# Performance work log

Measured on AMD Instinct MI355X. Metric: run time of the kernel, lower is better.

Reference implementation:

```python
import jax, jax.numpy as jnp
import numpy as np
from jax import lax

_A = -0.75  # PyTorch bicubic coefficient


def _cubic_kernel(x):
    x = np.abs(x)
    return np.where(x <= 1.0, (_A + 2) * x**3 - (_A + 3) * x**2 + 1,
                    np.where(x < 2.0, _A * x**3 - 5 * _A * x**2 + 8 * _A * x - 4 * _A, 0.0))


def _cubic_mat(out_s, in_s):
    # align_corners=True bicubic interpolation matrix [out_s, in_s]
    i = np.arange(out_s)
    s = i * (in_s - 1) / (out_s - 1) if out_s > 1 else np.zeros(out_s)
    f = np.floor(s).astype(np.int64)
    t = s - f
    M = np.zeros((out_s, in_s), dtype=np.float32)
    for off in range(-1, 3):
        idx = np.clip(f + off, 0, in_s - 1)
        np.add.at(M, (i, idx), _cubic_kernel(t - off).astype(np.float32))
    return jnp.asarray(M)


def _bicubic_up(x, out_hw):
    Mh = _cubic_mat(out_hw[0], x.shape[-2])
    Mw = _cubic_mat(out_hw[1], x.shape[-1])
    y = jnp.einsum('Hh,bchw->bcHw', Mh, x)
    return jnp.einsum('Ww,bcHw->bcHW', Mw, y)


def _conv(x, w, b, pad=1):
    y = lax.conv_general_dilated(x, w, (1, 1), [(pad, pad), (pad, pad)],
                                 dimension_numbers=('NCHW', 'OIHW', 'NCHW'))
    return y + b[None, :, None, None]


def _pool(x):
    return lax.reduce_window(x, -jnp.inf, lax.max, (1, 1, 2, 2), (1, 1, 2, 2), 'VALID')


def _features(x, ws):
    # VGG19 feat1 = conv0+relu (64ch, full res); feat2 = conv2..conv14 (256ch, 1/4 res)
    x1 = jax.nn.relu(_conv(x, *ws[0]))
    h = jax.nn.relu(_conv(x1, *ws[1]))
    h = _pool(h)
    h = jax.nn.relu(_conv(h, *ws[2]))
    h = jax.nn.relu(_conv(h, *ws[3]))
    h = _pool(h)
    h = jax.nn.relu(_conv(h, *ws[4]))
    h = jax.nn.relu(_conv(h, *ws[5]))
    h = jax.nn.relu(_conv(h, *ws[6]))
    h = _bicubic_up(h, x1.shape[-2:])  # bicubic, align_corners=True
    return jnp.concatenate([x1, h], axis=1)  # 64 + 256 = 320 channels


def _forward(x_ref, x_template, w0, b0, w2, b2, w5, b5, w7, b7, w10, b10, w12, b12,
             w14, b14, coef_ref, coef_temp, fw1, fb1, fw2, fb2, fw3, fb3):
    ws = [(w0, b0), (w2, b2), (w5, b5), (w7, b7), (w10, b10), (w12, b12), (w14, b14)]
    fref = _features(x_ref, ws)
    ftem = _features(x_template, ws)
    # L2-normalize over channel dim
    fref = fref / (1e-8 + jnp.linalg.norm(fref, axis=1, keepdims=True))
    ftem = ftem / (1e-8 + jnp.linalg.norm(ftem, axis=1, keepdims=True))
    b, c, H, W = fref.shape
    fref = fref.reshape(b, c, H // 2, 2, W // 2, 2).mean(axis=(3, 5))
    # dense correlation volume
    dist = jnp.einsum('bcmn,bcpq->bmnpq', fref, ftem) / 320.0
    m, n, p, q = dist.shape[1:]
    dist = dist.reshape(b, m * n, p * q)
    # dual-axis softmax + sqrt combination (LoFTR-style)
    conf_ref = jax.nn.softmax(coef_ref * dist, axis=-2)
    conf_tmp = jax.nn.softmax(coef_temp * dist, axis=-1)
    confidence = jnp.sqrt(conf_ref * conf_tmp)
    conf_values, _ = lax.top_k(confidence, 5)  # [b, m*n, 5]
    conf = conf_values.reshape(b, m, n, 5).transpose(0, 3, 1, 2)
    # final head (dropout = identity in eval)
    h = jax.nn.relu(_conv(conf, fw1, fb1))
    h = jax.nn.relu(_conv(h, fw2, fb2))
    out = _conv(h, fw3, fb3, pad=0)
    out = _bicubic_up(out, x_ref.shape[-2:])
    return out


def setup_inputs() -> dict:
    key = jax.random.key(0)
    ks = jax.random.split(key, 16)
    B, H, W = 1, 128, 128

    def cw(k, o, i, s):
        return jax.random.normal(k, (o, i, s, s), jnp.float32) * (1.0 / np.sqrt(i * s * s))

    d = {
        'x_ref': jax.random.normal(ks[0], (B, 3, H, W), jnp.float32),
        'x_template': jax.random.normal(ks[1], (B, 3, H, W), jnp.float32),
        'w0': cw(ks[2], 64, 3, 3), 'b0': jnp.zeros((64,), jnp.float32),
        'w2': cw(ks[3], 64, 64, 3), 'b2': jnp.zeros((64,), jnp.float32),
        'w5': cw(ks[4], 128, 64, 3), 'b5': jnp.zeros((128,), jnp.float32),
        'w7': cw(ks[5], 128, 128, 3), 'b7': jnp.zeros((128,), jnp.float32),
        'w10': cw(ks[6], 256, 128, 3), 'b10': jnp.zeros((256,), jnp.float32),
        'w12': cw(ks[7], 256, 256, 3), 'b12': jnp.zeros((256,), jnp.float32),
        'w14': cw(ks[8], 256, 256, 3), 'b14': jnp.zeros((256,), jnp.float32),
        'coef_ref': jnp.float32(1.0), 'coef_temp': jnp.float32(1.0),
        # final head: weights_init_normal -> N(1/3, 0.02)
        'fw1': 1.0 / 3 + 0.02 * jax.random.normal(ks[9], (8, 5, 3, 3), jnp.float32),
        'fb1': 0.02 * jax.random.normal(ks[10], (8,), jnp.float32),
        'fw2': 1.0 / 3 + 0.02 * jax.random.normal(ks[11], (8, 8, 3, 3), jnp.float32),
        'fb2': 0.02 * jax.random.normal(ks[12], (8,), jnp.float32),
        'fw3': 1.0 / 3 + 0.02 * jax.random.normal(ks[13], (1, 8, 1, 1), jnp.float32),
        'fb3': 0.02 * jax.random.normal(ks[14], (1,), jnp.float32),
    }
    return d


def reference(x_ref, x_template, w0, b0, w2, b2, w5, b5, w7, b7, w10, b10, w12, b12,
              w14, b14, coef_ref, coef_temp, fw1, fb1, fw2, fb2, fw3, fb3):
    return _forward(x_ref, x_template, w0, b0, w2, b2, w5, b5, w7, b7, w10, b10,
                    w12, b12, w14, b14, coef_ref, coef_temp, fw1, fb1, fw2, fb2, fw3, fb3)
```

## Files before the change

kernel.cpp:

```cpp
#include <hip/hip_runtime.h>
#include <math.h>

typedef unsigned short ushort_t;
typedef unsigned int uint_t;
typedef __attribute__((ext_vector_type(8))) short bf16x8;
typedef __attribute__((ext_vector_type(4))) float f32x4;

#define FSTRIDE ((size_t)16384 * 320)
#define TSTRIDE ((size_t)16384 * 64)

__device__ inline ushort_t f2bf(float f) {
    union { float f; uint_t u; } x; x.f = f;
    uint_t r = x.u + 0x7fffu + ((x.u >> 16) & 1u);
    return (ushort_t)(r >> 16);
}
__device__ inline float bf2f(ushort_t h) {
    union { uint_t u; float f; } x; x.u = ((uint_t)h) << 16;
    return x.f;
}
__device__ inline float bflo(uint_t u) {
    union { uint_t u; float f; } x; x.u = u << 16; return x.f;
}
__device__ inline float bfhi(uint_t u) {
    union { uint_t u; float f; } x; x.u = u & 0xffff0000u; return x.f;
}
__device__ inline uint_t cvtpk_bf16(float lo, float hi) {
    uint_t r;
    asm volatile("v_cvt_pk_bf16_f32 %0, %1, %2" : "=v"(r) : "v"(lo), "v"(hi));
    return r;
}
__device__ inline void gload16(const void* g, void* l) {
    __builtin_amdgcn_global_load_lds(
        (const __attribute__((address_space(1))) void*)g,
        (__attribute__((address_space(3))) void*)l, 16, 0, 0);
}

__global__ void wtrans_k(const float* __restrict__ w, ushort_t* __restrict__ wT, int CO, int CI)
{
    int idx = blockIdx.x * 256 + threadIdx.x;
    if (idx >= CO * CI * 9) return;
    int tap = idx % 9;
    int rem = idx / 9;
    int ci = rem % CI;
    int co = rem / CI;
    wT[((size_t)tap * CO + co) * CI + ci] = f2bf(w[idx]);
}

__global__ __launch_bounds__(256) void conv0_k(const float* __restrict__ x0, const float* __restrict__ x1,
                                               const float* __restrict__ w,
                                               const float* __restrict__ b, ushort_t* __restrict__ F)
{
    const float* x = blockIdx.y ? x1 : x0;
    F += (size_t)blockIdx.y * FSTRIDE;
    int co = threadIdx.x & 63;
    int p = blockIdx.x * 4 + (threadIdx.x >> 6);
    int y = p >> 7, xx = p & 127;
    float acc = b[co];
#pragma unroll
    for (int ci = 0; ci < 3; ++ci) {
#pragma unroll
        for (int t = 0; t < 9; ++t) {
            int dy = t / 3 - 1, dx = t % 3 - 1;
            int yy = y + dy, xc = xx + dx;
            if ((unsigned)yy < 128u && (unsigned)xc < 128u) {
                acc += x[ci * 16384 + yy * 128 + xc] * w[co * 27 + ci * 9 + t];
            }
        }
    }
    F[(size_t)p * 320 + co] = f2bf(fmaxf(acc, 0.f));
}

template<int CI>
__global__ __launch_bounds__(256) void conv_mfma_k(
    const ushort_t* __restrict__ in, int ldin, int inoff, size_t inImgStride,
    const ushort_t* __restrict__ wT, const float* __restrict__ bias,
    ushort_t* __restrict__ out, int ldout, int outoff, size_t outImgStride,
    int H, int W, int CO)
{
    in += (size_t)blockIdx.z * inImgStride;
    out += (size_t)blockIdx.z * outImgStride;
    const int tid = threadIdx.x;
    const int lane = tid & 63, wid = tid >> 6;
    const int wr = wid >> 1, wc = wid & 1;
    const int m0 = blockIdx.x * 64;
    const int n0 = blockIdx.y * 64;
    const int fr = lane & 15;
    const int fo = (lane >> 4) << 3;

    size_t abase[2];
    unsigned vmask[2];
#pragma unroll
    for (int mi = 0; mi < 2; ++mi) {
        int p = m0 + wr * 32 + mi * 16 + fr;
        int y = p / W, x = p % W;
        abase[mi] = (size_t)p * ldin + inoff + fo;
        unsigned vm = 0;
#pragma unroll
        for (int t = 0; t < 9; ++t) {
            int dy = t / 3 - 1, dx = t % 3 - 1;
            if ((unsigned)(y + dy) < (unsigned)H && (unsigned)(x + dx) < (unsigned)W) vm |= 1u << t;
        }
        vmask[mi] = vm;
    }

    f32x4 zero = {0.f, 0.f, 0.f, 0.f};
    f32x4 acc[2][2] = {{zero, zero}, {zero, zero}};
    const bf16x8 zz = {0, 0, 0, 0, 0, 0, 0, 0};

    for (int t = 0; t < 9; ++t) {
        int toff = ((t / 3 - 1) * W + (t % 3 - 1)) * ldin;
        bool v0 = (vmask[0] >> t) & 1u;
        bool v1 = (vmask[1] >> t) & 1u;
        const ushort_t* wp0 = wT + ((size_t)(t * CO + n0 + wc * 32 + fr)) * CI + fo;
        const ushort_t* wp1 = wp0 + (size_t)16 * CI;
#pragma unroll
        for (int kc = 0; kc < CI / 32; ++kc) {
            int k0 = kc * 32;
            bf16x8 a0 = v0 ? *(const bf16x8*)(in + abase[0] + toff + k0) : zz;
            bf16x8 a1 = v1 ? *(const bf16x8*)(in + abase[1] + toff + k0) : zz;
            bf16x8 b0 = *(const bf16x8*)(wp0 + k0);
            bf16x8 b1 = *(const bf16x8*)(wp1 + k0);
            acc[0][0] = __builtin_amdgcn_mfma_f32_16x16x32_bf16(b0, a0, acc[0][0], 0, 0, 0);
            acc[0][1] = __builtin_amdgcn_mfma_f32_16x16x32_bf16(b1, a0, acc[0][1], 0, 0, 0);
            acc[1][0] = __builtin_amdgcn_mfma_f32_16x16x32_bf16(b0, a1, acc[1][0], 0, 0, 0);
            acc[1][1] = __builtin_amdgcn_mfma_f32_16x16x32_bf16(b1, a1, acc[1][1], 0, 0, 0);
        }
    }

#pragma unroll
    for (int mi = 0; mi < 2; ++mi) {
#pragma unroll
        for (int ni = 0; ni < 2; ++ni) {
            int pix = m0 + wr * 32 + mi * 16 + (lane & 15);
            int ch = n0 + wc * 32 + ni * 16 + ((lane >> 4) << 2);
            float4 bv = *(const float4*)(bias + ch);
            float r0 = fmaxf(acc[mi][ni][0] + bv.x, 0.f);
            float r1 = fmaxf(acc[mi][ni][1] + bv.y, 0.f);
            float r2 = fmaxf(acc[mi][ni][2] + bv.z, 0.f);
            float r3 = fmaxf(acc[mi][ni][3] + bv.w, 0.f);
            uint2 pk;
            pk.x = (uint_t)f2bf(r0) | ((uint_t)f2bf(r1) << 16);
            pk.y = (uint_t)f2bf(r2) | ((uint_t)f2bf(r3) << 16);
            *(uint2*)(out + (size_t)pix * ldout + outoff + ch) = pk;
        }
    }
}

template<int CI>
__global__ __launch_bounds__(64) void conv_mfma1w_k(
    const ushort_t* __restrict__ in, int ldin, size_t inImgStride,
    const ushort_t* __restrict__ wT, const float* __restrict__ bias,
    ushort_t* __restrict__ out, int ldout, size_t outImgStride,
    int H, int W, int CO)
{
    in += (size_t)blockIdx.z * inImgStride;
    out += (size_t)blockIdx.z * outImgStride;
    const int lane = threadIdx.x;
    const int m0 = blockIdx.x * 32;
    const int n0 = blockIdx.y * 32;
    const int fr = lane & 15;
    const int fo = (lane >> 4) << 3;

    size_t abase[2];
    unsigned vmask[2];
#pragma unroll
    for (int mi = 0; mi < 2; ++mi) {
        int p = m0 + mi * 16 + fr;
        int y = p / W, x = p % W;
        abase[mi] = (size_t)p * ldin + fo;
        unsigned vm = 0;
#pragma unroll
        for (int t = 0; t < 9; ++t) {
            int dy = t / 3 - 1, dx = t % 3 - 1;
            if ((unsigned)(y + dy) < (unsigned)H && (unsigned)(x + dx) < (unsigned)W) vm |= 1u << t;
        }
        vmask[mi] = vm;
    }

    f32x4 zero = {0.f, 0.f, 0.f, 0.f};
    f32x4 acc[2][2] = {{zero, zero}, {zero, zero}};
    const bf16x8 zz = {0, 0, 0, 0, 0, 0, 0, 0};

    for (int t = 0; t < 9; ++t) {
        int toff = ((t / 3 - 1) * W + (t % 3 - 1)) * ldin;
        bool v0 = (vmask[0] >> t) & 1u;
        bool v1 = (vmask[1] >> t) & 1u;
        const ushort_t* wp0 = wT + ((size_t)(t * CO + n0 + fr)) * CI + fo;
        const ushort_t* wp1 = wp0 + (size_t)16 * CI;
#pragma unroll
        for (int kc = 0; kc < CI / 32; ++kc) {
            int k0 = kc * 32;
            bf16x8 a0 = v0 ? *(const bf16x8*)(in + abase[0] + toff + k0) : zz;
            bf16x8 a1 = v1 ? *(const bf16x8*)(in + abase[1] + toff + k0) : zz;
            bf16x8 b0 = *(const bf16x8*)(wp0 + k0);
            bf16x8 b1 = *(const bf16x8*)(wp1 + k0);
            acc[0][0] = __builtin_amdgcn_mfma_f32_16x16x32_bf16(b0, a0, acc[0][0], 0, 0, 0);
            acc[0][1] = __builtin_amdgcn_mfma_f32_16x16x32_bf16(b1, a0, acc[0][1], 0, 0, 0);
            acc[1][0] = __builtin_amdgcn_mfma_f32_16x16x32_bf16(b0, a1, acc[1][0], 0, 0, 0);
            acc[1][1] = __builtin_amdgcn_mfma_f32_16x16x32_bf16(b1, a1, acc[1][1], 0, 0, 0);
        }
    }

#pragma unroll
    for (int mi = 0; mi < 2; ++mi) {
#pragma unroll
        for (int ni = 0; ni < 2; ++ni) {
            int pix = m0 + mi * 16 + (lane & 15);
            int ch = n0 + ni * 16 + ((lane >> 4) << 2);
            float4 bv = *(const float4*)(bias + ch);
            float r0 = fmaxf(acc[mi][ni][0] + bv.x, 0.f);
            float r1 = fmaxf(acc[mi][ni][1] + bv.y, 0.f);
            float r2 = fmaxf(acc[mi][ni][2] + bv.z, 0.f);
            float r3 = fmaxf(acc[mi][ni][3] + bv.w, 0.f);
            uint2 pk;
            pk.x = (uint_t)f2bf(r0) | ((uint_t)f2bf(r1) << 16);
            pk.y = (uint_t)f2bf(r2) | ((uint_t)f2bf(r3) << 16);
            *(uint2*)(out + (size_t)pix * ldout + ch) = pk;
        }
    }
}

__global__ void maxpool_nhwc_k(const ushort_t* __restrict__ in, ushort_t* __restrict__ out,
                               int C, int Hi, int Wi)
{
    in += (size_t)blockIdx.y * TSTRIDE;
    out += (size_t)blockIdx.y * TSTRIDE;
    int idx = blockIdx.x * 256 + threadIdx.x;
    int CG = C >> 3;
    int Wo = Wi >> 1, Ho = Hi >> 1;
    if (idx >= Ho * Wo * CG) return;
    int cg = idx % CG;
    int p = idx / CG;
    int y = p / Wo, x = p % Wo;
    const ushort_t* ip = in + ((size_t)(2 * y) * Wi + 2 * x) * C + cg * 8;
    bf16x8 v0 = *(const bf16x8*)(ip);
    bf16x8 v1 = *(const bf16x8*)(ip + C);
    bf16x8 v2 = *(const bf16x8*)(ip + (size_t)Wi * C);
    bf16x8 v3 = *(const bf16x8*)(ip + (size_t)Wi * C + C);
    bf16x8 r;
#pragma unroll
    for (int j = 0; j < 8; ++j) {
        float m = fmaxf(fmaxf(bf2f((ushort_t)v0[j]), bf2f((ushort_t)v1[j])),
                        fmaxf(bf2f((ushort_t)v2[j]), bf2f((ushort_t)v3[j])));
        r[j] = (short)f2bf(m);
    }
    *(bf16x8*)(out + (size_t)p * C + cg * 8) = r;
}

__device__ inline void cubw(float t, float* w) {
    float x0 = 1.f + t, x2 = 1.f - t, x3 = 2.f - t;
    w[0] = ((-0.75f*x0 + 3.75f)*x0 - 6.f)*x0 + 3.f;
    w[1] = (1.25f*t - 2.25f)*t*t + 1.f;
    w[2] = (1.25f*x2 - 2.25f)*x2*x2 + 1.f;
    w[3] = ((-0.75f*x3 + 3.75f)*x3 - 6.f)*x3 + 3.f;
}

__global__ __launch_bounds__(256) void bicubic_nhwc_k(const ushort_t* __restrict__ in, ushort_t* __restrict__ F)
{
    in += (size_t)blockIdx.y * TSTRIDE;
    F += (size_t)blockIdx.y * FSTRIDE;
    int idx = blockIdx.x * 256 + threadIdx.x;
    int cg = idx & 31;
    int p = idx >> 5;
    int Y = p >> 7, X = p & 127;
    float sy = (float)Y * (31.f / 127.f);
    float sx = (float)X * (31.f / 127.f);
    int fy = (int)floorf(sy), fx = (int)floorf(sx);
    float ty = sy - (float)fy, tx = sx - (float)fx;
    float wy[4], wx[4];
    cubw(ty, wy); cubw(tx, wx);
    float a[8] = {0.f, 0.f, 0.f, 0.f, 0.f, 0.f, 0.f, 0.f};
#pragma unroll
    for (int i = 0; i < 4; ++i) {
        int yy = min(max(fy - 1 + i, 0), 31);
#pragma unroll
        for (int j = 0; j < 4; ++j) {
            int xx = min(max(fx - 1 + j, 0), 31);
            float w = wy[i] * wx[j];
            bf16x8 v = *(const bf16x8*)(in + ((size_t)yy * 32 + xx) * 256 + cg * 8);
#pragma unroll
            for (int e = 0; e < 8; ++e) a[e] += w * bf2f((ushort_t)v[e]);
        }
    }
    bf16x8 r;
#pragma unroll
    for (int e = 0; e < 8; ++e) r[e] = (short)f2bf(a[e]);
    *(bf16x8*)(F + (size_t)p * 320 + 64 + cg * 8) = r;
}

__global__ __launch_bounds__(256) void norm_k(ushort_t* __restrict__ F)
{
    int lane = threadIdx.x & 63;
    int p = blockIdx.x * 4 + (threadIdx.x >> 6);
    ushort_t* rp = F + (size_t)p * 320;
    bool act = lane < 40;
    bf16x8 v = {0, 0, 0, 0, 0, 0, 0, 0};
    float ss = 0.f;
    if (act) {
        v = *(const bf16x8*)(rp + lane * 8);
#pragma unroll
        for (int e = 0; e < 8; ++e) { float f = bf2f((ushort_t)v[e]); ss += f * f; }
    }
#pragma unroll
    for (int off = 32; off > 0; off >>= 1) ss += __shfl_xor(ss, off);
    float inv = 1.f / (1e-8f + sqrtf(ss));
    if (act) {
#pragma unroll
        for (int e = 0; e < 8; ++e) v[e] = (short)f2bf(bf2f((ushort_t)v[e]) * inv);
        *(bf16x8*)(rp + lane * 8) = v;
    }
}

__global__ void pool_ref_nhwc_k(const ushort_t* __restrict__ F, ushort_t* __restrict__ A)
{
    int idx = blockIdx.x * 256 + threadIdx.x;
    if (idx >= 4096 * 40) return;
    int cg = idx % 40;
    int m = idx / 40;
    int y = m >> 6, x = m & 63;
    const ushort_t* ip = F + ((size_t)(2 * y) * 128 + 2 * x) * 320 + cg * 8;
    bf16x8 v0 = *(const bf16x8*)(ip);
    bf16x8 v1 = *(const bf16x8*)(ip + 320);
    bf16x8 v2 = *(const bf16x8*)(ip + 128 * 320);
    bf16x8 v3 = *(const bf16x8*)(ip + 128 * 320 + 320);
    bf16x8 r;
#pragma unroll
    for (int j = 0; j < 8; ++j) {
        float s = bf2f((ushort_t)v0[j]) + bf2f((ushort_t)v1[j]) + bf2f((ushort_t)v2[j]) + bf2f((ushort_t)v3[j]);
        r[j] = (short)f2bf(0.25f * s);
    }
    *(bf16x8*)(A + (size_t)m * 320 + cg * 8) = r;
}

__global__ __launch_bounds__(256) void gemm_corr_k(
    const ushort_t* __restrict__ A, const ushort_t* __restrict__ B, ushort_t* __restrict__ D,
    const float* __restrict__ coefr, const float* __restrict__ coeft,
    float* __restrict__ rpsum, float* __restrict__ cpsum)
{
    __shared__ ushort_t lA[128 * 32];
    __shared__ ushort_t lB[128 * 32];
    __shared__ float cl[2][128];
    __shared__ float rl[2][128];
    const int tid = threadIdx.x;
    const int lane = tid & 63;
    const int wid = tid >> 6;
    const int wr = wid >> 1, wc = wid & 1;
    const int m0 = blockIdx.y * 128, n0 = blockIdx.x * 128;
    const int fr = lane & 15;
    const int fo = (lane >> 4) << 3;
    const int srow = tid >> 2;
    const int scol = (tid & 3) << 3;

    const ushort_t* Ag0 = A + (size_t)(m0 + srow) * 320 + scol;
    const ushort_t* Ag1 = Ag0 + (size_t)64 * 320;
    const ushort_t* Bg0 = B + (size_t)(n0 + srow) * 320 + scol;
    const ushort_t* Bg1 = Bg0 + (size_t)64 * 320;
    ushort_t* lA0 = lA + wid * 512;
    ushort_t* lA1 = lA + 2048 + wid * 512;
    ushort_t* lB0 = lB + wid * 512;
    ushort_t* lB1 = lB + 2048 + wid * 512;

    f32x4 zero = {0.f, 0.f, 0.f, 0.f};
    f32x4 acc[4][4];
#pragma unroll
    for (int i = 0; i < 4; ++i)
#pragma unroll
        for (int j = 0; j < 4; ++j) acc[i][j] = zero;

    for (int k0 = 0; k0 < 320; k0 += 32) {
        gload16(Ag0 + k0, lA0);
        gload16(Ag1 + k0, lA1);
        gload16(Bg0 + k0, lB0);
        gload16(Bg1 + k0, lB1);
        __syncthreads();
        bf16x8 af[4], bfr[4];
#pragma unroll
        for (int mi = 0; mi < 4; ++mi)
            af[mi] = *(const bf16x8*)&lA[(wr * 64 + mi * 16 + fr) * 32 + fo];
#pragma unroll
        for (int ni = 0; ni < 4; ++ni)
            bfr[ni] = *(const bf16x8*)&lB[(wc * 64 + ni * 16 + fr) * 32 + fo];
#pragma unroll
        for (int mi = 0; mi < 4; ++mi)
#pragma unroll
            for (int ni = 0; ni < 4; ++ni)
                acc[mi][ni] = __builtin_amdgcn_mfma_f32_16x16x32_bf16(bfr[ni], af[mi], acc[mi][ni], 0, 0, 0);
        __syncthreads();
    }

    const float s = 1.0f / 320.0f;
    const float cr = coefr[0], ct = coeft[0];
    const bool sameCoef = (cr == ct);
    float rpx[4] = {0.f, 0.f, 0.f, 0.f};
    float cpx[4][4];
#pragma unroll
    for (int ni = 0; ni < 4; ++ni)
#pragma unroll
        for (int r = 0; r < 4; ++r) cpx[ni][r] = 0.f;

    const int mrow = lane & 15;
    const int ng = (lane >> 4) << 2;
#pragma unroll
    for (int mi = 0; mi < 4; ++mi) {
        int m = m0 + wr * 64 + mi * 16 + mrow;
        ushort_t* drow = D + (size_t)m * 16384;
#pragma unroll
        for (int ni = 0; ni < 4; ++ni) {
            int n = n0 + wc * 64 + ni * 16 + ng;
            float d0 = acc[mi][ni][0] * s;
            float d1 = acc[mi][ni][1] * s;
            float d2 = acc[mi][ni][2] * s;
            float d3 = acc[mi][ni][3] * s;
            uint2 pk;
            pk.x = cvtpk_bf16(d0, d1);
            pk.y = cvtpk_bf16(d2, d3);
            *(uint2*)(drow + n) = pk;
            float e0 = __expf(cr * d0), e1 = __expf(cr * d1);
            float e2 = __expf(cr * d2), e3 = __expf(cr * d3);
            cpx[ni][0] += e0; cpx[ni][1] += e1; cpx[ni][2] += e2; cpx[ni][3] += e3;
            if (sameCoef) {
                rpx[mi] += e0 + e1 + e2 + e3;
            } else {
                rpx[mi] += __expf(ct * d0) + __expf(ct * d1) + __expf(ct * d2) + __expf(ct * d3);
            }
        }
    }
#pragma unroll
    for (int mi = 0; mi < 4; ++mi) {
        rpx[mi] += __shfl_xor(rpx[mi], 16);
        rpx[mi] += __shfl_xor(rpx[mi], 32);
    }
    if (lane < 16) {
#pragma unroll
        for (int mi = 0; mi < 4; ++mi)
            rl[wc][wr * 64 + mi * 16 + lane] = rpx[mi];
    }
#pragma unroll
    for (int ni = 0; ni < 4; ++ni)
#pragma unroll
        for (int r = 0; r < 4; ++r) {
            cpx[ni][r] += __shfl_xor(cpx[ni][r], 1);
            cpx[ni][r] += __shfl_xor(cpx[ni][r], 2);
            cpx[ni][r] += __shfl_xor(cpx[ni][r], 4);
            cpx[ni][r] += __shfl_xor(cpx[ni][r], 8);
        }
    if ((lane & 15) == 0) {
        int g = lane >> 4;
#pragma unroll
        for (int ni = 0; ni < 4; ++ni)
#pragma unroll
            for (int r = 0; r < 4; ++r)
                cl[wr][wc * 64 + ni * 16 + g * 4 + r] = cpx[ni][r];
    }
    __syncthreads();
    if (tid < 128) {
        cpsum[(size_t)blockIdx.y * 16384 + n0 + tid] = cl[0][tid] + cl[1][tid];
        rpsum[(size_t)blockIdx.x * 4096 + m0 + tid] = rl[0][tid] + rl[1][tid];
    }
}

__global__ void colfin_k(const float* __restrict__ cpsum, float* __restrict__ lc)
{
    int j = blockIdx.x * 256 + threadIdx.x;
    float s = 0.f;
#pragma unroll
    for (int k = 0; k < 32; ++k) s += cpsum[(size_t)k * 16384 + j];
    lc[j] = -0.5f * __logf(s);
}
__global__ void rowfin_k(const float* __restrict__ rpsum, float* __restrict__ invr)
{
    int m = blockIdx.x * 256 + threadIdx.x;
    float s = 0.f;
#pragma unroll
    for (int k = 0; k < 128; ++k) s += rpsum[(size_t)k * 4096 + m];
    invr[m] = rsqrtf(s);
}

#define INS5(w_) { float w = (w_); float mx; \
    mx = fmaxf(w, t0); w = fminf(w, t0); t0 = mx; \
    mx = fmaxf(w, t1); w = fminf(w, t1); t1 = mx; \
    mx = fmaxf(w, t2); w = fminf(w, t2); t2 = mx; \
    mx = fmaxf(w, t3); w = fminf(w, t3); t3 = mx; \
    t4 = fmaxf(w, t4); }

__global__ __launch_bounds__(256) void row_topk_k(
    const ushort_t* __restrict__ Dist, const float* __restrict__ lc,
    const float* __restrict__ invr,
    const float* __restrict__ coefr, const float* __restrict__ coeft,
    float* __restrict__ conf5)
{
    int wid = threadIdx.x >> 6, lane = threadIdx.x & 63;
    int row = blockIdx.x * 4 + wid;
    float hc = 0.5f * (coefr[0] + coeft[0]);
    const ushort_t* rp = Dist + (size_t)row * 16384;

    float t0 = -1e30f, t1 = -1e30f, t2 = -1e30f, t3 = -1e30f, t4 = -1e30f;
    for (int i = 0; i < 32; ++i) {
        int col = (i * 64 + lane) * 8;
        uint4 u = *(const uint4*)(rp + col);
        float4 l0 = *(const float4*)(lc + col);
        float4 l1 = *(const float4*)(lc + col + 4);
        INS5(fmaf(hc, bflo(u.x), l0.x));
        INS5(fmaf(hc, bfhi(u.x), l0.y));
        INS5(fmaf(hc, bflo(u.y), l0.z));
        INS5(fmaf(hc, bfhi(u.y), l0.w));
        INS5(fmaf(hc, bflo(u.z), l1.x));
        INS5(fmaf(hc, bfhi(u.z), l1.y));
        INS5(fmaf(hc, bflo(u.w), l1.z));
        INS5(fmaf(hc, bfhi(u.w), l1.w));
    }
#pragma unroll
    for (int off = 1; off < 64; off <<= 1) {
        float o0 = __shfl_xor(t0, off), o1 = __shfl_xor(t1, off), o2 = __shfl_xor(t2, off);
        float o3 = __shfl_xor(t3, off), o4 = __shfl_xor(t4, off);
        INS5(o0); INS5(o1); INS5(o2); INS5(o3); INS5(o4);
    }
    if (lane == 0) {
        float iv = invr[row];
        conf5[0 * 4096 + row] = __expf(t0) * iv;
        conf5[1 * 4096 + row] = __expf(t1) * iv;
        conf5[2 * 4096 + row] = __expf(t2) * iv;
        conf5[3 * 4096 + row] = __expf(t3) * iv;
        conf5[4 * 4096 + row] = __expf(t4) * iv;
    }
}

__global__ void conv3x3_k(const float* __restrict__ in, const float* __restrict__ wgt,
                          const float* __restrict__ bias, float* __restrict__ out,
                          int Cin, int H, int W, int relu)
{
    int p = blockIdx.x * 256 + threadIdx.x;
    int HW = H * W;
    if (p >= HW) return;
    int co0 = blockIdx.y * 8;
    int y = p / W, x = p - y * W;
    float acc0 = bias[co0+0], acc1 = bias[co0+1], acc2 = bias[co0+2], acc3 = bias[co0+3];
    float acc4 = bias[co0+4], acc5 = bias[co0+5], acc6 = bias[co0+6], acc7 = bias[co0+7];
    bool ym = y > 0, yp = y < H-1, xm = x > 0, xp = x < W-1;
    for (int ci = 0; ci < Cin; ++ci) {
        const float* ip = in + (size_t)ci * HW + p;
        float v0 = (ym && xm) ? ip[-W-1] : 0.f;
        float v1 = (ym)       ? ip[-W]   : 0.f;
        float v2 = (ym && xp) ? ip[-W+1] : 0.f;
        float v3 = (xm)       ? ip[-1]   : 0.f;
        float v4 =              ip[0];
        float v5 = (xp)       ? ip[1]    : 0.f;
        float v6 = (yp && xm) ? ip[W-1]  : 0.f;
        float v7 = (yp)       ? ip[W]    : 0.f;
        float v8 = (yp && xp) ? ip[W+1]  : 0.f;
        const float* wp = wgt + ((size_t)co0 * Cin + ci) * 9;
        size_t ws = (size_t)Cin * 9;
#define CACC(q, a) { const float* wq = wp + q * ws; \
        a += wq[0]*v0 + wq[1]*v1 + wq[2]*v2 + wq[3]*v3 + wq[4]*v4 \
           + wq[5]*v5 + wq[6]*v6 + wq[7]*v7 + wq[8]*v8; }
        CACC(0, acc0) CACC(1, acc1) CACC(2, acc2) CACC(3, acc3)
        CACC(4, acc4) CACC(5, acc5) CACC(6, acc6) CACC(7, acc7)
#undef CACC
    }
#define CW(q, a) { float r = a; if (relu) r = fmaxf(r, 0.f); out[(size_t)(co0+q)*HW + p] = r; }
    CW(0, acc0) CW(1, acc1) CW(2, acc2) CW(3, acc3)
    CW(4, acc4) CW(5, acc5) CW(6, acc6) CW(7, acc7)
#undef CW
}

__global__ void bicubic_k(const float* __restrict__ in, float* __restrict__ out,
                          int C, int Hin, int Win, int Hout, int Wout)
{
    int idx = blockIdx.x * 256 + threadIdx.x;
    int total = C * Hout * Wout;
    if (idx >= total) return;
    int X = idx % Wout;
    int Y = (idx / Wout) % Hout;
    int c = idx / (Wout * Hout);
    float sy = (float)Y * (float)(Hin - 1) / (float)(Hout - 1);
    float sx = (float)X * (float)(Win - 1) / (float)(Wout - 1);
    int fy = (int)floorf(sy), fx = (int)floorf(sx);
    float ty = sy - (float)fy, tx = sx - (float)fx;
    float wy[4], wx[4];
    cubw(ty, wy); cubw(tx, wx);
    const float* ip = in + (size_t)c * Hin * Win;
    float acc = 0.f;
#pragma unroll
    for (int i = 0; i < 4; ++i) {
        int yy = min(max(fy - 1 + i, 0), Hin - 1);
        float ra = 0.f;
#pragma unroll
        for (int j = 0; j < 4; ++j) {
            int xx = min(max(fx - 1 + j, 0), Win - 1);
            ra += wx[j] * ip[yy * Win + xx];
        }
        acc += wy[i] * ra;
    }
    out[idx] = acc;
}

__global__ void conv1x1_k(const float* __restrict__ in, const float* __restrict__ w,
                          const float* __restrict__ b, float* __restrict__ out, int Cin, int HW)
{
    int p = blockIdx.x * 256 + threadIdx.x;
    if (p >= HW) return;
    float a = b[0];
    for (int c = 0; c < Cin; ++c) a += w[c] * in[(size_t)c * HW + p];
    out[p] = a;
}

extern "C" void kernel_launch(void* const* d_in, const int* in_sizes, int n_in,
                              void* d_out, int out_size, void* d_ws, size_t ws_size,
                              hipStream_t stream)
{
    const float* x_ref = (const float*)d_in[0];
    const float* x_tem = (const float*)d_in[1];
    const float* w0  = (const float*)d_in[2];   const float* b0  = (const float*)d_in[3];
    const float* w2  = (const float*)d_in[4];   const float* b2  = (const float*)d_in[5];
    const float* w5  = (const float*)d_in[6];   const float* b5  = (const float*)d_in[7];
    const float* w7  = (const float*)d_in[8];   const float* b7  = (const float*)d_in[9];
    const float* w10 = (const float*)d_in[10];  const float* b10 = (const float*)d_in[11];
    const float* w12 = (const float*)d_in[12];  const float* b12 = (const float*)d_in[13];
    const float* w14 = (const float*)d_in[14];  const float* b14 = (const float*)d_in[15];
    const float* coefr = (const float*)d_in[16];
    const float* coeft = (const float*)d_in[17];
    const float* fw1 = (const float*)d_in[18];  const float* fb1 = (const float*)d_in[19];
    const float* fw2 = (const float*)d_in[20];  const float* fb2 = (const float*)d_in[21];
    const float* fw3 = (const float*)d_in[22];  const float* fb3 = (const float*)d_in[23];
    float* out = (float*)d_out;

    char* wsp = (char*)d_ws;
    auto alloc = [&](size_t bytes) { char* p = wsp; wsp += (bytes + 255) & ~(size_t)255; return p; };
    ushort_t* F     = (ushort_t*)alloc(2 * FSTRIDE * 2);
    ushort_t* t1    = (ushort_t*)alloc(2 * TSTRIDE * 2);
    ushort_t* t2    = (ushort_t*)alloc(2 * TSTRIDE * 2);
    ushort_t* wT2   = (ushort_t*)alloc((size_t)64 * 64 * 9 * 2);
    ushort_t* wT5   = (ushort_t*)alloc((size_t)128 * 64 * 9 * 2);
    ushort_t* wT7   = (ushort_t*)alloc((size_t)128 * 128 * 9 * 2);
    ushort_t* wT10  = (ushort_t*)alloc((size_t)256 * 128 * 9 * 2);
    ushort_t* wT12  = (ushort_t*)alloc((size_t)256 * 256 * 9 * 2);
    ushort_t* wT14  = (ushort_t*)alloc((size_t)256 * 256 * 9 * 2);
    ushort_t* Abuf  = (ushort_t*)alloc((size_t)4096 * 320 * 2);
    ushort_t* dist  = (ushort_t*)alloc((size_t)4096 * 16384 * 2);
    float*    rpsum = (float*)alloc((size_t)128 * 4096 * 4);
    float*    cpsum = (float*)alloc((size_t)32 * 16384 * 4);
    float*    lc    = (float*)alloc(16384 * 4);
    float*    invr  = (float*)alloc(4096 * 4);
    float*    conf5 = (float*)alloc(5 * 4096 * 4);
    float*    h1    = (float*)alloc(8 * 4096 * 4);
    float*    h2    = (float*)alloc(8 * 4096 * 4);
    float*    out64 = (float*)alloc(4096 * 4);
    (void)ws_size; (void)n_in; (void)in_sizes; (void)out_size;

    wtrans_k<<<(64*64*9 + 255)/256, 256, 0, stream>>>(w2, wT2, 64, 64);
    wtrans_k<<<(128*64*9 + 255)/256, 256, 0, stream>>>(w5, wT5, 128, 64);
    wtrans_k<<<(128*128*9 + 255)/256, 256, 0, stream>>>(w7, wT7, 128, 128);
    wtrans_k<<<(256*128*9 + 255)/256, 256, 0, stream>>>(w10, wT10, 256, 128);
    wtrans_k<<<(256*256*9 + 255)/256, 256, 0, stream>>>(w12, wT12, 256, 256);
    wtrans_k<<<(256*256*9 + 255)/256, 256, 0, stream>>>(w14, wT14, 256, 256);

    conv0_k<<<dim3(4096, 2), 256, 0, stream>>>(x_ref, x_tem, w0, b0, F);
    conv_mfma_k<64><<<dim3(256, 1, 2), 256, 0, stream>>>(F, 320, 0, FSTRIDE, wT2, b2, t1, 64, 0, TSTRIDE, 128, 128, 64);
    maxpool_nhwc_k<<<dim3(128, 2), 256, 0, stream>>>(t1, t2, 64, 128, 128);
    conv_mfma_k<64><<<dim3(64, 2, 2), 256, 0, stream>>>(t2, 64, 0, TSTRIDE, wT5, b5, t1, 128, 0, TSTRIDE, 64, 64, 128);
    conv_mfma_k<128><<<dim3(64, 2, 2), 256, 0, stream>>>(t1, 128, 0, TSTRIDE, wT7, b7, t2, 128, 0, TSTRIDE, 64, 64, 128);
    maxpool_nhwc_k<<<dim3(64, 2), 256, 0, stream>>>(t2, t1, 128, 64, 64);
    conv_mfma1w_k<128><<<dim3(32, 8, 2), 64, 0, stream>>>(t1, 128, TSTRIDE, wT10, b10, t2, 256, TSTRIDE, 32, 32, 256);
    conv_mfma1w_k<256><<<dim3(32, 8, 2), 64, 0, stream>>>(t2, 256, TSTRIDE, wT12, b12, t1, 256, TSTRIDE, 32, 32, 256);
    conv_mfma1w_k<256><<<dim3(32, 8, 2), 64, 0, stream>>>(t1, 256, TSTRIDE, wT14, b14, t2, 256, TSTRIDE, 32, 32, 256);
    bicubic_nhwc_k<<<dim3(2048, 2), 256, 0, stream>>>(t2, F);
    norm_k<<<8192, 256, 0, stream>>>(F);

    pool_ref_nhwc_k<<<640, 256, 0, stream>>>(F, Abuf);

    gemm_corr_k<<<dim3(128, 32), 256, 0, stream>>>(Abuf, F + FSTRIDE, dist, coefr, coeft, rpsum, cpsum);

    colfin_k<<<64, 256, 0, stream>>>(cpsum, lc);
    rowfin_k<<<16, 256, 0, stream>>>(rpsum, invr);

    row_topk_k<<<1024, 256, 0, stream>>>(dist, lc, invr, coefr, coeft, conf5);

    conv3x3_k<<<dim3(16, 1), 256, 0, stream>>>(conf5, fw1, fb1, h1, 5, 64, 64, 1);
    conv3x3_k<<<dim3(16, 1), 256, 0, stream>>>(h1, fw2, fb2, h2, 8, 64, 64, 1);
    conv1x1_k<<<16, 256, 0, stream>>>(h2, fw3, fb3, out64, 8, 4096);
    bicubic_k<<<64, 256, 0, stream>>>(out64, out, 1, 64, 64, 128, 128);
}
```

Baseline: 409.7 us.

## Double-buffer LDS in correlation GEMM and early-skip top-5 insertion in row scan

The correlation GEMM now uses two LDS buffers per operand and issues the global-to-LDS loads for the next K slice before running MFMAs on the current one. This removes one barrier per iteration and lets load latency overlap with compute, at the cost of doubling that kernel's shared memory. The row top-5 kernel first takes the max of each group of 8 candidates and skips the insertion network when that max cannot beat the current 5th best. Most groups should then need only a few compares instead of 8 insertions, though the new branch can diverge across lanes.

```diff
diff --git a/kernel.cpp b/kernel.cpp
--- a/kernel.cpp
+++ b/kernel.cpp
@@ -337,8 +337,8 @@
     const float* __restrict__ coefr, const float* __restrict__ coeft,
     float* __restrict__ rpsum, float* __restrict__ cpsum)
 {
-    __shared__ ushort_t lA[128 * 32];
-    __shared__ ushort_t lB[128 * 32];
+    __shared__ ushort_t lA[2][128 * 32];
+    __shared__ ushort_t lB[2][128 * 32];
     __shared__ float cl[2][128];
     __shared__ float rl[2][128];
     const int tid = threadIdx.x;
@@ -355,10 +355,6 @@
     const ushort_t* Ag1 = Ag0 + (size_t)64 * 320;
     const ushort_t* Bg0 = B + (size_t)(n0 + srow) * 320 + scol;
     const ushort_t* Bg1 = Bg0 + (size_t)64 * 320;
-    ushort_t* lA0 = lA + wid * 512;
-    ushort_t* lA1 = lA + 2048 + wid * 512;
-    ushort_t* lB0 = lB + wid * 512;
-    ushort_t* lB1 = lB + 2048 + wid * 512;
 
     f32x4 zero = {0.f, 0.f, 0.f, 0.f};
     f32x4 acc[4][4];
@@ -367,26 +363,38 @@
 #pragma unroll
         for (int j = 0; j < 4; ++j) acc[i][j] = zero;
 
-    for (int k0 = 0; k0 < 320; k0 += 32) {
-        gload16(Ag0 + k0, lA0);
-        gload16(Ag1 + k0, lA1);
-        gload16(Bg0 + k0, lB0);
-        gload16(Bg1 + k0, lB1);
+#define STAGE(buf, k0) { \
+        gload16(Ag0 + (k0), &lA[buf][wid * 512]); \
+        gload16(Ag1 + (k0), &lA[buf][2048 + wid * 512]); \
+        gload16(Bg0 + (k0), &lB[buf][wid * 512]); \
+        gload16(Bg1 + (k0), &lB[buf][2048 + wid * 512]); }
+
+#define COMPUTE(buf) { \
+        bf16x8 af[4], bfr[4]; \
+        _Pragma("unroll") \
+        for (int mi = 0; mi < 4; ++mi) \
+            af[mi] = *(const bf16x8*)&lA[buf][(wr * 64 + mi * 16 + fr) * 32 + fo]; \
+        _Pragma("unroll") \
+        for (int ni = 0; ni < 4; ++ni) \
+            bfr[ni] = *(const bf16x8*)&lB[buf][(wc * 64 + ni * 16 + fr) * 32 + fo]; \
+        _Pragma("unroll") \
+        for (int mi = 0; mi < 4; ++mi) \
+            _Pragma("unroll") \
+            for (int ni = 0; ni < 4; ++ni) \
+                acc[mi][ni] = __builtin_amdgcn_mfma_f32_16x16x32_bf16(bfr[ni], af[mi], acc[mi][ni], 0, 0, 0); }
+
+    int cur = 0;
+    STAGE(0, 0)
+    __syncthreads();
+    for (int k0 = 32; k0 < 320; k0 += 32) {
+        STAGE(cur ^ 1, k0)
+        COMPUTE(cur)
         __syncthreads();
-        bf16x8 af[4], bfr[4];
-#pragma unroll
-        for (int mi = 0; mi < 4; ++mi)
-            af[mi] = *(const bf16x8*)&lA[(wr * 64 + mi * 16 + fr) * 32 + fo];
-#pragma unroll
-        for (int ni = 0; ni < 4; ++ni)
-            bfr[ni] = *(const bf16x8*)&lB[(wc * 64 + ni * 16 + fr) * 32 + fo];
-#pragma unroll
-        for (int mi = 0; mi < 4; ++mi)
-#pragma unroll
-            for (int ni = 0; ni < 4; ++ni)
-                acc[mi][ni] = __builtin_amdgcn_mfma_f32_16x16x32_bf16(bfr[ni], af[mi], acc[mi][ni], 0, 0, 0);
-        __syncthreads();
-    }
+        cur ^= 1;
+    }
+    COMPUTE(cur)
+#undef STAGE
+#undef COMPUTE
 
     const float s = 1.0f / 320.0f;
     const float cr = coefr[0], ct = coeft[0];
@@ -500,14 +508,20 @@
         uint4 u = *(const uint4*)(rp + col);
         float4 l0 = *(const float4*)(lc + col);
         float4 l1 = *(const float4*)(lc + col + 4);
-        INS5(fmaf(hc, bflo(u.x), l0.x));
-        INS5(fmaf(hc, bfhi(u.x), l0.y));
-        INS5(fmaf(hc, bflo(u.y), l0.z));
-        INS5(fmaf(hc, bfhi(u.y), l0.w));
-        INS5(fmaf(hc, bflo(u.z), l1.x));
-        INS5(fmaf(hc, bfhi(u.z), l1.y));
-        INS5(fmaf(hc, bflo(u.w), l1.z));
-        INS5(fmaf(hc, bfhi(u.w), l1.w));
+        float k0 = fmaf(hc, bflo(u.x), l0.x);
+        float k1 = fmaf(hc, bfhi(u.x), l0.y);
+        float k2 = fmaf(hc, bflo(u.y), l0.z);
+        float k3 = fmaf(hc, bfhi(u.y), l0.w);
+        float k4 = fmaf(hc, bflo(u.z), l1.x);
+        float k5 = fmaf(hc, bfhi(u.z), l1.y);
+        float k6 = fmaf(hc, bflo(u.w), l1.z);
+        float k7 = fmaf(hc, bfhi(u.w), l1.w);
+        float m8 = fmaxf(fmaxf(fmaxf(k0, k1), fmaxf(k2, k3)),
+                         fmaxf(fmaxf(k4, k5), fmaxf(k6, k7)));
+        if (m8 > t4) {
+            INS5(k0); INS5(k1); INS5(k2); INS5(k3);
+            INS5(k4); INS5(k5); INS5(k6); INS5(k7);
+        }
     }
 #pragma unroll
     for (int off = 1; off < 64; off <<= 1) {
```

After: 417.0 us. About the same (+1.8%).
